# Kernel tuning notes

Measured on AMD Instinct MI355X. Metric: run time of the kernel, lower is better.

Reference implementation:

```python
import jax, jax.numpy as jnp
import numpy as np

B = 65536       # batch size
C = 100         # num classes (len(cls_num_list))
ALPHA = 0.01    # soft-label blend weight
TAU = 2.0       # init arg tau
TEMP = 2.0      # distillation temperature
EPS = 1e-9


def _soft_ce(logits, soft_targets):
    # -(soft * log softmax(logits)).sum(1).mean()
    return -(soft_targets * jax.nn.log_softmax(logits, axis=1)).sum(axis=1).mean()


def _inverse_prior(prior):
    idx0 = jnp.argsort(prior)            # ascending sort permutation
    value = prior[idx0]                  # sorted values
    idx1 = jnp.argsort(idx0)             # rank of each element
    idx2 = prior.shape[0] - 1 - idx1     # mirrored rank
    return value[idx2]


def setup_inputs():
    key = jax.random.key(0)
    ks = jax.random.split(key, 8)
    cls_num = np.arange(500, 0, -5).astype(np.float32)  # matches init cls_num_list
    prior = jnp.asarray(cls_num / cls_num.sum(), dtype=jnp.float32)
    return {
        "output_logits": jax.random.normal(ks[0], (B, C), jnp.float32),
        "target": jax.random.randint(ks[1], (B,), 0, C),
        "cos_feature": jax.random.normal(ks[2], (C, C), jnp.float32),
        "old_pred": jax.random.normal(ks[3], (B, C), jnp.float32),
        "expert1_logits": jax.random.normal(ks[4], (B, C), jnp.float32),
        "expert2_logits": jax.random.normal(ks[5], (B, C), jnp.float32),
        "expert3_logits": jax.random.normal(ks[6], (B, C), jnp.float32),
        "output": jax.random.normal(ks[7], (B, C), jnp.float32),
        "prior": prior,
        "epoch": 5,
    }


def reference(output_logits, target, cos_feature, old_pred, expert1_logits,
              expert2_logits, expert3_logits, output, prior, epoch):
    num_classes = prior.shape[0]
    # ---- convert_to_soft_labels (vectorized: gather rows of sim matrix, softmax, blend) ----
    one_hot = jax.nn.one_hot(target, num_classes, dtype=jnp.float32)          # [B,C]
    sim_probs = jax.nn.softmax(cos_feature, axis=1)[target]                   # [B,C]
    label = (1.0 - ALPHA) * one_hot + ALPHA * sim_probs

    # ---- three expert soft cross-entropies ----
    log_prior = jnp.log(prior + EPS)
    loss = _soft_ce(expert1_logits, label)
    loss = loss + _soft_ce(expert2_logits + log_prior, label)
    inv_prior = _inverse_prior(prior)
    loss = loss + _soft_ce(expert3_logits + log_prior - TAU * jnp.log(inv_prior + EPS), label)

    # ---- bincount-normalized summed logits ----
    counts = jnp.bincount(target, length=num_classes).astype(jnp.float32)     # [C]
    num = counts[target][:, None]                                             # [B,1]
    expert_sum_logits = output / num                                          # [B,C]

    # ---- masked KL distillation (only rows where teacher argmax == target) ----
    teacher_index = jnp.argmax(old_pred, axis=1)                              # argmax(softmax)=argmax
    mask = (teacher_index == target).astype(jnp.float32)                      # [B]
    t = jax.nn.softmax(old_pred / TEMP, axis=1)                               # teacher probs
    s = jax.nn.log_softmax(expert_sum_logits / TEMP, axis=1)                  # student log-probs
    log_t = jnp.where(t > 0, jnp.log(t), 0.0)
    kl_per = (t * (log_t - s)).sum(axis=1)                                    # [B] per-row KL
    n_sel = mask.sum()
    kl_loss = jnp.where(n_sel > 0, (kl_per * mask).sum() / jnp.maximum(n_sel, 1.0), 0.0)
    kl_loss = kl_loss * (TEMP ** 2) * 3.0

    return loss, kl_loss, expert_sum_logits
```

## Files before the change

### kernel.cpp

```cpp
#include <hip/hip_runtime.h>
#include <math.h>

#define B_N 65536
#define C_N 100
constexpr float ALPHA = 0.01f;
constexpr float TAU   = 2.0f;
constexpr float TEMP  = 2.0f;
constexpr float EPSF  = 1e-9f;
constexpr float NEG_SENT = -1.0e30f;

template<int CTRL>
__device__ __forceinline__ float fadd_dpp(float x) {
    return x + __int_as_float(__builtin_amdgcn_update_dpp(
        0, __float_as_int(x), CTRL, 0xF, 0xF, true));
}
__device__ __forceinline__ float rowsum32(float x) {
    x = fadd_dpp<0xB1>(x);
    x = fadd_dpp<0x4E>(x);
    x = fadd_dpp<0x124>(x);
    x = fadd_dpp<0x128>(x);
    x = fadd_dpp<0x142>(x);
    return x;
}
template<int CTRL>
__device__ __forceinline__ void amax_dpp(unsigned &hi, unsigned &lo) {
    const unsigned yh = (unsigned)__builtin_amdgcn_update_dpp(0, (int)hi, CTRL, 0xF, 0xF, true);
    const unsigned yl = (unsigned)__builtin_amdgcn_update_dpp(0, (int)lo, CTRL, 0xF, 0xF, true);
    const bool take = (yh > hi) || (yh == hi && yl > lo);
    hi = take ? yh : hi;
    lo = take ? yl : lo;
}
__device__ __forceinline__ void rowamax32(unsigned &hi, unsigned &lo) {
    amax_dpp<0xB1>(hi, lo);
    amax_dpp<0x4E>(hi, lo);
    amax_dpp<0x124>(hi, lo);
    amax_dpp<0x128>(hi, lo);
    amax_dpp<0x142>(hi, lo);
}

__device__ __forceinline__ float wsum(float v) {
    #pragma unroll
    for (int o = 32; o; o >>= 1) v += __shfl_xor(v, o);
    return v;
}

__global__ void prep_k(const float* __restrict__ cosf, const float* __restrict__ prior,
                       const int* __restrict__ target,
                       float* __restrict__ sm, float* __restrict__ lp, float* __restrict__ c3,
                       int* __restrict__ counts) {
    const int b = blockIdx.x;
    if (b < 256) {
        __shared__ int h[C_N];
        for (int i = threadIdx.x; i < C_N; i += blockDim.x) h[i] = 0;
        __syncthreads();
        const int gid = b * blockDim.x + threadIdx.x;
        const int stride = 256 * blockDim.x;
        for (int i = gid; i < B_N; i += stride) atomicAdd(&h[target[i]], 1);
        __syncthreads();
        for (int i = threadIdx.x; i < C_N; i += blockDim.x)
            if (h[i]) atomicAdd(&counts[i], h[i]);
    } else if (b == 256) {
        __shared__ float sp[C_N];
        __shared__ float val[C_N];
        const int t = threadIdx.x;
        if (t < C_N) sp[t] = prior[t];
        __syncthreads();
        int rank = 0;
        float lpi = 0.f;
        if (t < C_N) {
            const float pi = sp[t];
            for (int j = 0; j < C_N; ++j) {
                const float pj = sp[j];
                rank += (pj < pi) || (pj == pi && j < t);
            }
            val[rank] = pi;
            lpi = __logf(pi + EPSF);
            lp[t] = lpi;
        }
        __syncthreads();
        if (t < C_N) {
            const float inv = val[C_N - 1 - rank];
            c3[t] = lpi - TAU * __logf(inv + EPSF);
        }
    } else {
        const int gw = (b - 257) * 4 + (threadIdx.x >> 6);
        const int lane = threadIdx.x & 63;
        for (int row = gw; row < C_N; row += 16) {
            const float* rp = cosf + row * C_N;
            const float v0 = rp[lane];
            const bool has1 = (lane + 64) < C_N;
            const float v1 = has1 ? rp[lane + 64] : -INFINITY;
            float m = fmaxf(v0, v1);
            #pragma unroll
            for (int o = 32; o; o >>= 1) m = fmaxf(m, __shfl_xor(m, o));
            const float e0 = __expf(v0 - m);
            const float e1 = has1 ? __expf(v1 - m) : 0.f;
            const float s = wsum(e0 + e1);
            const float is = 1.0f / s;
            sm[row * C_N + lane] = e0 * is;
            if (has1) sm[row * C_N + lane + 64] = e1 * is;
        }
    }
}

#define NBLK 4096

__launch_bounds__(256)
__global__ void main_k(const int* __restrict__ target,
                       const float* __restrict__ e1p, const float* __restrict__ e2p,
                       const float* __restrict__ e3p, const float* __restrict__ opp,
                       const float* __restrict__ outp,
                       const float* __restrict__ sm, const float* __restrict__ lp,
                       const float* __restrict__ c3, const int* __restrict__ counts,
                       float* __restrict__ dout,
                       float* __restrict__ ploss, float* __restrict__ pkl, float* __restrict__ pn) {
    const int lane = threadIdx.x & 63;
    const int gl   = lane & 31;
    const int half = lane >> 5;
    const int wslot = threadIdx.x >> 6;
    const int gw   = blockIdx.x * 4 + wslot;
    const bool act = gl < 25;
    const int c0 = 4 * gl;
    const bool own = (gl == 16);

    const int rowA = 4 * gw + half;
    const int rowB = 4 * gw + 2 + half;
    const int tgtA = target[rowA];
    const int tgtB = target[rowB];
    const int baseA = rowA * C_N;
    const int baseB = rowB * C_N;

    float4 LP = make_float4(0,0,0,0), CO = make_float4(0,0,0,0);
    float4 E1A, E2A, E3A, OPA, OUA, SMA, E1B, E2B, E3B, OPB, OUB, SMB;
    E1A = E2A = E3A = OPA = OUA = make_float4(NEG_SENT, NEG_SENT, NEG_SENT, NEG_SENT);
    E1B = E2B = E3B = OPB = OUB = make_float4(NEG_SENT, NEG_SENT, NEG_SENT, NEG_SENT);
    SMA = SMB = make_float4(0,0,0,0);
    if (act) {
        LP  = *(const float4*)(lp + c0);
        CO  = *(const float4*)(c3 + c0);
        E1A = *(const float4*)(e1p + baseA + c0);
        E1B = *(const float4*)(e1p + baseB + c0);
        E2A = *(const float4*)(e2p + baseA + c0);
        E2B = *(const float4*)(e2p + baseB + c0);
        E3A = *(const float4*)(e3p + baseA + c0);
        E3B = *(const float4*)(e3p + baseB + c0);
        OPA = *(const float4*)(opp + baseA + c0);
        OPB = *(const float4*)(opp + baseB + c0);
        OUA = *(const float4*)(outp + baseA + c0);
        OUB = *(const float4*)(outp + baseB + c0);
        SMA = *(const float4*)(sm + tgtA * C_N + c0);
        SMB = *(const float4*)(sm + tgtB * C_N + c0);
    }
    const float rcA = 1.0f / (float)counts[tgtA];
    const float rcB = 1.0f / (float)counts[tgtB];

    const float laA0 = (1.0f - ALPHA) * (c0     == tgtA) + ALPHA * SMA.x;
    const float laA1 = (1.0f - ALPHA) * (c0 + 1 == tgtA) + ALPHA * SMA.y;
    const float laA2 = (1.0f - ALPHA) * (c0 + 2 == tgtA) + ALPHA * SMA.z;
    const float laA3 = (1.0f - ALPHA) * (c0 + 3 == tgtA) + ALPHA * SMA.w;
    const float lA20 = E2A.x + LP.x, lA21 = E2A.y + LP.y, lA22 = E2A.z + LP.z, lA23 = E2A.w + LP.w;
    const float lA30 = E3A.x + CO.x, lA31 = E3A.y + CO.y, lA32 = E3A.z + CO.z, lA33 = E3A.w + CO.w;
    float s1A = __expf(E1A.x) + __expf(E1A.y) + __expf(E1A.z) + __expf(E1A.w);
    float s2A = __expf(lA20) + __expf(lA21) + __expf(lA22) + __expf(lA23);
    float s3A = __expf(lA30) + __expf(lA31) + __expf(lA32) + __expf(lA33);
    float dtA = laA0 * (E1A.x + lA20 + lA30) + laA1 * (E1A.y + lA21 + lA31)
              + laA2 * (E1A.z + lA22 + lA32) + laA3 * (E1A.w + lA23 + lA33);
    const float aA0 = OPA.x * 0.5f, aA1 = OPA.y * 0.5f, aA2 = OPA.z * 0.5f, aA3 = OPA.w * 0.5f;
    const float pA0 = __expf(aA0), pA1 = __expf(aA1), pA2 = __expf(aA2), pA3 = __expf(aA3);
    float ztA = pA0 + pA1 + pA2 + pA3;
    float bvA = OPA.x; int biA = c0;
    if (OPA.y > bvA) { bvA = OPA.y; biA = c0 + 1; }
    if (OPA.z > bvA) { bvA = OPA.z; biA = c0 + 2; }
    if (OPA.w > bvA) { bvA = OPA.w; biA = c0 + 3; }
    unsigned bbA = __float_as_uint(bvA);
    bbA = ((int)bbA < 0) ? ~bbA : (bbA | 0x80000000u);
    unsigned khiA = bbA, kloA = (unsigned)~biA;
    const float esA0 = OUA.x * rcA, esA1 = OUA.y * rcA, esA2 = OUA.z * rcA, esA3 = OUA.w * rcA;
    const float xA0 = esA0 * 0.5f, xA1 = esA1 * 0.5f, xA2 = esA2 * 0.5f, xA3 = esA3 * 0.5f;
    float zsA = __expf(xA0) + __expf(xA1) + __expf(xA2) + __expf(xA3);
    float DA  = pA0 * (aA0 - xA0) + pA1 * (aA1 - xA1) + pA2 * (aA2 - xA2) + pA3 * (aA3 - xA3);
    if (act) {
        *(float2*)(dout + 2 + baseA + c0)     = make_float2(esA0, esA1);
        *(float2*)(dout + 2 + baseA + c0 + 2) = make_float2(esA2, esA3);
    }

    const float laB0 = (1.0f - ALPHA) * (c0     == tgtB) + ALPHA * SMB.x;
    const float laB1 = (1.0f - ALPHA) * (c0 + 1 == tgtB) + ALPHA * SMB.y;
    const float laB2 = (1.0f - ALPHA) * (c0 + 2 == tgtB) + ALPHA * SMB.z;
    const float laB3 = (1.0f - ALPHA) * (c0 + 3 == tgtB) + ALPHA * SMB.w;
    const float lB20 = E2B.x + LP.x, lB21 = E2B.y + LP.y, lB22 = E2B.z + LP.z, lB23 = E2B.w + LP.w;
    const float lB30 = E3B.x + CO.x, lB31 = E3B.y + CO.y, lB32 = E3B.z + CO.z, lB33 = E3B.w + CO.w;
    float s1B = __expf(E1B.x) + __expf(E1B.y) + __expf(E1B.z) + __expf(E1B.w);
    float s2B = __expf(lB20) + __expf(lB21) + __expf(lB22) + __expf(lB23);
    float s3B = __expf(lB30) + __expf(lB31) + __expf(lB32) + __expf(lB33);
    float dtB = laB0 * (E1B.x + lB20 + lB30) + laB1 * (E1B.y + lB21 + lB31)
              + laB2 * (E1B.z + lB22 + lB32) + laB3 * (E1B.w + lB23 + lB33);
    const float aB0 = OPB.x * 0.5f, aB1 = OPB.y * 0.5f, aB2 = OPB.z * 0.5f, aB3 = OPB.w * 0.5f;
    const float pB0 = __expf(aB0), pB1 = __expf(aB1), pB2 = __expf(aB2), pB3 = __expf(aB3);
    float ztB = pB0 + pB1 + pB2 + pB3;
    float bvB = OPB.x; int biB = c0;
    if (OPB.y > bvB) { bvB = OPB.y; biB = c0 + 1; }
    if (OPB.z > bvB) { bvB = OPB.z; biB = c0 + 2; }
    if (OPB.w > bvB) { bvB = OPB.w; biB = c0 + 3; }
    unsigned bbB = __float_as_uint(bvB);
    bbB = ((int)bbB < 0) ? ~bbB : (bbB | 0x80000000u);
    unsigned khiB = bbB, kloB = (unsigned)~biB;
    const float esB0 = OUB.x * rcB, esB1 = OUB.y * rcB, esB2 = OUB.z * rcB, esB3 = OUB.w * rcB;
    const float xB0 = esB0 * 0.5f, xB1 = esB1 * 0.5f, xB2 = esB2 * 0.5f, xB3 = esB3 * 0.5f;
    float zsB = __expf(xB0) + __expf(xB1) + __expf(xB2) + __expf(xB3);
    float DB  = pB0 * (aB0 - xB0) + pB1 * (aB1 - xB1) + pB2 * (aB2 - xB2) + pB3 * (aB3 - xB3);
    if (act) {
        *(float2*)(dout + 2 + baseB + c0)     = make_float2(esB0, esB1);
        *(float2*)(dout + 2 + baseB + c0 + 2) = make_float2(esB2, esB3);
    }

    s1A = rowsum32(s1A);  s1B = rowsum32(s1B);
    s2A = rowsum32(s2A);  s2B = rowsum32(s2B);
    s3A = rowsum32(s3A);  s3B = rowsum32(s3B);
    dtA = rowsum32(dtA);  dtB = rowsum32(dtB);
    ztA = rowsum32(ztA);  ztB = rowsum32(ztB);
    zsA = rowsum32(zsA);  zsB = rowsum32(zsB);
    DA  = rowsum32(DA);   DB  = rowsum32(DB);
    rowamax32(khiA, kloA);
    rowamax32(khiB, kloB);

    const float ceA = __logf(s1A * s2A * s3A) - dtA;
    const float ceB = __logf(s1B * s2B * s3B) - dtB;
    const int miA = (int)~kloA;
    const int miB = (int)~kloB;
    const float rztA = 1.0f / ztA, rztB = 1.0f / ztB;
    const float klvA = DA * rztA + __logf(zsA * rztA);
    const float klvB = DB * rztB + __logf(zsB * rztB);
    const bool selA = own && (miA == tgtA);
    const bool selB = own && (miB == tgtB);

    float lossAcc = own ? (ceA + ceB) : 0.f;
    float klAcc   = (selA ? klvA : 0.f) + (selB ? klvB : 0.f);
    float nAcc    = (selA ? 1.f : 0.f) + (selB ? 1.f : 0.f);

    const float lossW = __shfl(lossAcc, 16) + __shfl(lossAcc, 48);
    const float klW   = __shfl(klAcc, 16) + __shfl(klAcc, 48);
    const float nW    = __shfl(nAcc, 16) + __shfl(nAcc, 48);

    __shared__ float bl[4], bk[4], bn[4];
    if (lane == 0) { bl[wslot] = lossW; bk[wslot] = klW; bn[wslot] = nW; }
    __syncthreads();
    if (threadIdx.x == 0) {
        ploss[blockIdx.x] = bl[0] + bl[1] + bl[2] + bl[3];
        pkl[blockIdx.x]   = bk[0] + bk[1] + bk[2] + bk[3];
        pn[blockIdx.x]    = bn[0] + bn[1] + bn[2] + bn[3];
    }
}

__global__ void final_k(const float* __restrict__ ploss, const float* __restrict__ pkl,
                        const float* __restrict__ pn, float* __restrict__ dout) {
    __shared__ float sl[256], sk[256], sn[256];
    const int t = threadIdx.x;
    float l = 0.f, k = 0.f, n = 0.f;
    for (int i = t; i < NBLK; i += 256) { l += ploss[i]; k += pkl[i]; n += pn[i]; }
    sl[t] = l; sk[t] = k; sn[t] = n;
    __syncthreads();
    for (int s = 128; s; s >>= 1) {
        if (t < s) { sl[t] += sl[t + s]; sk[t] += sk[t + s]; sn[t] += sn[t + s]; }
        __syncthreads();
    }
    if (t == 0) {
        dout[0] = sl[0] / (float)B_N;
        const float kl = (sn[0] > 0.f) ? (sk[0] / fmaxf(sn[0], 1.f)) : 0.f;
        dout[1] = kl * (TEMP * TEMP) * 3.0f;
    }
}

extern "C" void kernel_launch(void* const* d_in, const int* in_sizes, int n_in,
                              void* d_out, int out_size, void* d_ws, size_t ws_size,
                              hipStream_t stream) {
    const int*   target = (const int*)  d_in[1];
    const float* cosf   = (const float*)d_in[2];
    const float* oldp   = (const float*)d_in[3];
    const float* e1     = (const float*)d_in[4];
    const float* e2     = (const float*)d_in[5];
    const float* e3     = (const float*)d_in[6];
    const float* outp   = (const float*)d_in[7];
    const float* prior  = (const float*)d_in[8];

    float* ws    = (float*)d_ws;
    float* sm    = ws;
    float* lp    = ws + 10000;
    float* c3    = ws + 10100;
    int*   cnts  = (int*)(ws + 10200);
    float* ploss = ws + 10304;
    float* pkl   = ploss + NBLK;
    float* pn    = pkl + NBLK;

    hipMemsetAsync(cnts, 0, C_N * sizeof(int), stream);
    prep_k<<<261, 256, 0, stream>>>(cosf, prior, target, sm, lp, c3, cnts);
    main_k<<<NBLK, 256, 0, stream>>>(target, e1, e2, e3, oldp, outp,
                                     sm, lp, c3, cnts, (float*)d_out, ploss, pkl, pn);
    final_k<<<1, 256, 0, stream>>>(ploss, pkl, pn, (float*)d_out);
}
```

Before: 52.45 us.

## Split main kernel into CE and KL block halves and fold prior biases into weights

The fused per-row kernel becomes two block populations. The first half of the grid computes the three soft cross-entropies and the second half computes the masked KL and writes the normalized logits. Each block therefore holds fewer live registers and loads fewer streams, which should raise occupancy and memory-level parallelism. The prior offsets are also folded algebraically into precomputed multiplicative weights (exp of the bias) and a combined additive term, removing per-element adds. The costs are twice as many blocks, each reloading target, and slightly different floating-point rounding from exp(x)*w instead of exp(x+log w).

```diff
diff --git a/kernel.cpp b/kernel.cpp
--- a/kernel.cpp
+++ b/kernel.cpp
@@ -46,7 +46,8 @@
 
 __global__ void prep_k(const float* __restrict__ cosf, const float* __restrict__ prior,
                        const int* __restrict__ target,
-                       float* __restrict__ sm, float* __restrict__ lp, float* __restrict__ c3,
+                       float* __restrict__ sm, float* __restrict__ w2,
+                       float* __restrict__ w3, float* __restrict__ Ht,
                        int* __restrict__ counts) {
     const int b = blockIdx.x;
     if (b < 256) {
@@ -66,21 +67,23 @@
         if (t < C_N) sp[t] = prior[t];
         __syncthreads();
         int rank = 0;
-        float lpi = 0.f;
+        float lpi = 0.f, pi = 0.f;
         if (t < C_N) {
-            const float pi = sp[t];
+            pi = sp[t];
             for (int j = 0; j < C_N; ++j) {
                 const float pj = sp[j];
                 rank += (pj < pi) || (pj == pi && j < t);
             }
             val[rank] = pi;
             lpi = __logf(pi + EPSF);
-            lp[t] = lpi;
         }
         __syncthreads();
         if (t < C_N) {
             const float inv = val[C_N - 1 - rank];
-            c3[t] = lpi - TAU * __logf(inv + EPSF);
+            const float c3v = lpi - TAU * __logf(inv + EPSF);
+            w2[t] = pi + EPSF;
+            w3[t] = __expf(c3v);
+            Ht[t] = lpi + c3v;
         }
     } else {
         const int gw = (b - 257) * 4 + (threadIdx.x >> 6);
@@ -103,152 +106,176 @@
     }
 }
 
-#define NBLK 4096
+#define HBLK 4096
+#define NBLK (2 * HBLK)
 
 __launch_bounds__(256)
 __global__ void main_k(const int* __restrict__ target,
                        const float* __restrict__ e1p, const float* __restrict__ e2p,
                        const float* __restrict__ e3p, const float* __restrict__ opp,
                        const float* __restrict__ outp,
-                       const float* __restrict__ sm, const float* __restrict__ lp,
-                       const float* __restrict__ c3, const int* __restrict__ counts,
+                       const float* __restrict__ sm, const float* __restrict__ w2p,
+                       const float* __restrict__ w3p, const float* __restrict__ Hp,
+                       const int* __restrict__ counts,
                        float* __restrict__ dout,
                        float* __restrict__ ploss, float* __restrict__ pkl, float* __restrict__ pn) {
     const int lane = threadIdx.x & 63;
     const int gl   = lane & 31;
     const int half = lane >> 5;
     const int wslot = threadIdx.x >> 6;
-    const int gw   = blockIdx.x * 4 + wslot;
     const bool act = gl < 25;
     const int c0 = 4 * gl;
     const bool own = (gl == 16);
-
-    const int rowA = 4 * gw + half;
-    const int rowB = 4 * gw + 2 + half;
-    const int tgtA = target[rowA];
-    const int tgtB = target[rowB];
-    const int baseA = rowA * C_N;
-    const int baseB = rowB * C_N;
-
-    float4 LP = make_float4(0,0,0,0), CO = make_float4(0,0,0,0);
-    float4 E1A, E2A, E3A, OPA, OUA, SMA, E1B, E2B, E3B, OPB, OUB, SMB;
-    E1A = E2A = E3A = OPA = OUA = make_float4(NEG_SENT, NEG_SENT, NEG_SENT, NEG_SENT);
-    E1B = E2B = E3B = OPB = OUB = make_float4(NEG_SENT, NEG_SENT, NEG_SENT, NEG_SENT);
-    SMA = SMB = make_float4(0,0,0,0);
-    if (act) {
-        LP  = *(const float4*)(lp + c0);
-        CO  = *(const float4*)(c3 + c0);
-        E1A = *(const float4*)(e1p + baseA + c0);
-        E1B = *(const float4*)(e1p + baseB + c0);
-        E2A = *(const float4*)(e2p + baseA + c0);
-        E2B = *(const float4*)(e2p + baseB + c0);
-        E3A = *(const float4*)(e3p + baseA + c0);
-        E3B = *(const float4*)(e3p + baseB + c0);
-        OPA = *(const float4*)(opp + baseA + c0);
-        OPB = *(const float4*)(opp + baseB + c0);
-        OUA = *(const float4*)(outp + baseA + c0);
-        OUB = *(const float4*)(outp + baseB + c0);
-        SMA = *(const float4*)(sm + tgtA * C_N + c0);
-        SMB = *(const float4*)(sm + tgtB * C_N + c0);
-    }
-    const float rcA = 1.0f / (float)counts[tgtA];
-    const float rcB = 1.0f / (float)counts[tgtB];
-
-    const float laA0 = (1.0f - ALPHA) * (c0     == tgtA) + ALPHA * SMA.x;
-    const float laA1 = (1.0f - ALPHA) * (c0 + 1 == tgtA) + ALPHA * SMA.y;
-    const float laA2 = (1.0f - ALPHA) * (c0 + 2 == tgtA) + ALPHA * SMA.z;
-    const float laA3 = (1.0f - ALPHA) * (c0 + 3 == tgtA) + ALPHA * SMA.w;
-    const float lA20 = E2A.x + LP.x, lA21 = E2A.y + LP.y, lA22 = E2A.z + LP.z, lA23 = E2A.w + LP.w;
-    const float lA30 = E3A.x + CO.x, lA31 = E3A.y + CO.y, lA32 = E3A.z + CO.z, lA33 = E3A.w + CO.w;
-    float s1A = __expf(E1A.x) + __expf(E1A.y) + __expf(E1A.z) + __expf(E1A.w);
-    float s2A = __expf(lA20) + __expf(lA21) + __expf(lA22) + __expf(lA23);
-    float s3A = __expf(lA30) + __expf(lA31) + __expf(lA32) + __expf(lA33);
-    float dtA = laA0 * (E1A.x + lA20 + lA30) + laA1 * (E1A.y + lA21 + lA31)
-              + laA2 * (E1A.z + lA22 + lA32) + laA3 * (E1A.w + lA23 + lA33);
-    const float aA0 = OPA.x * 0.5f, aA1 = OPA.y * 0.5f, aA2 = OPA.z * 0.5f, aA3 = OPA.w * 0.5f;
-    const float pA0 = __expf(aA0), pA1 = __expf(aA1), pA2 = __expf(aA2), pA3 = __expf(aA3);
-    float ztA = pA0 + pA1 + pA2 + pA3;
-    float bvA = OPA.x; int biA = c0;
-    if (OPA.y > bvA) { bvA = OPA.y; biA = c0 + 1; }
-    if (OPA.z > bvA) { bvA = OPA.z; biA = c0 + 2; }
-    if (OPA.w > bvA) { bvA = OPA.w; biA = c0 + 3; }
-    unsigned bbA = __float_as_uint(bvA);
-    bbA = ((int)bbA < 0) ? ~bbA : (bbA | 0x80000000u);
-    unsigned khiA = bbA, kloA = (unsigned)~biA;
-    const float esA0 = OUA.x * rcA, esA1 = OUA.y * rcA, esA2 = OUA.z * rcA, esA3 = OUA.w * rcA;
-    const float xA0 = esA0 * 0.5f, xA1 = esA1 * 0.5f, xA2 = esA2 * 0.5f, xA3 = esA3 * 0.5f;
-    float zsA = __expf(xA0) + __expf(xA1) + __expf(xA2) + __expf(xA3);
-    float DA  = pA0 * (aA0 - xA0) + pA1 * (aA1 - xA1) + pA2 * (aA2 - xA2) + pA3 * (aA3 - xA3);
-    if (act) {
-        *(float2*)(dout + 2 + baseA + c0)     = make_float2(esA0, esA1);
-        *(float2*)(dout + 2 + baseA + c0 + 2) = make_float2(esA2, esA3);
-    }
-
-    const float laB0 = (1.0f - ALPHA) * (c0     == tgtB) + ALPHA * SMB.x;
-    const float laB1 = (1.0f - ALPHA) * (c0 + 1 == tgtB) + ALPHA * SMB.y;
-    const float laB2 = (1.0f - ALPHA) * (c0 + 2 == tgtB) + ALPHA * SMB.z;
-    const float laB3 = (1.0f - ALPHA) * (c0 + 3 == tgtB) + ALPHA * SMB.w;
-    const float lB20 = E2B.x + LP.x, lB21 = E2B.y + LP.y, lB22 = E2B.z + LP.z, lB23 = E2B.w + LP.w;
-    const float lB30 = E3B.x + CO.x, lB31 = E3B.y + CO.y, lB32 = E3B.z + CO.z, lB33 = E3B.w + CO.w;
-    float s1B = __expf(E1B.x) + __expf(E1B.y) + __expf(E1B.z) + __expf(E1B.w);
-    float s2B = __expf(lB20) + __expf(lB21) + __expf(lB22) + __expf(lB23);
-    float s3B = __expf(lB30) + __expf(lB31) + __expf(lB32) + __expf(lB33);
-    float dtB = laB0 * (E1B.x + lB20 + lB30) + laB1 * (E1B.y + lB21 + lB31)
-              + laB2 * (E1B.z + lB22 + lB32) + laB3 * (E1B.w + lB23 + lB33);
-    const float aB0 = OPB.x * 0.5f, aB1 = OPB.y * 0.5f, aB2 = OPB.z * 0.5f, aB3 = OPB.w * 0.5f;
-    const float pB0 = __expf(aB0), pB1 = __expf(aB1), pB2 = __expf(aB2), pB3 = __expf(aB3);
-    float ztB = pB0 + pB1 + pB2 + pB3;
-    float bvB = OPB.x; int biB = c0;
-    if (OPB.y > bvB) { bvB = OPB.y; biB = c0 + 1; }
-    if (OPB.z > bvB) { bvB = OPB.z; biB = c0 + 2; }
-    if (OPB.w > bvB) { bvB = OPB.w; biB = c0 + 3; }
-    unsigned bbB = __float_as_uint(bvB);
-    bbB = ((int)bbB < 0) ? ~bbB : (bbB | 0x80000000u);
-    unsigned khiB = bbB, kloB = (unsigned)~biB;
-    const float esB0 = OUB.x * rcB, esB1 = OUB.y * rcB, esB2 = OUB.z * rcB, esB3 = OUB.w * rcB;
-    const float xB0 = esB0 * 0.5f, xB1 = esB1 * 0.5f, xB2 = esB2 * 0.5f, xB3 = esB3 * 0.5f;
-    float zsB = __expf(xB0) + __expf(xB1) + __expf(xB2) + __expf(xB3);
-    float DB  = pB0 * (aB0 - xB0) + pB1 * (aB1 - xB1) + pB2 * (aB2 - xB2) + pB3 * (aB3 - xB3);
-    if (act) {
-        *(float2*)(dout + 2 + baseB + c0)     = make_float2(esB0, esB1);
-        *(float2*)(dout + 2 + baseB + c0 + 2) = make_float2(esB2, esB3);
-    }
-
-    s1A = rowsum32(s1A);  s1B = rowsum32(s1B);
-    s2A = rowsum32(s2A);  s2B = rowsum32(s2B);
-    s3A = rowsum32(s3A);  s3B = rowsum32(s3B);
-    dtA = rowsum32(dtA);  dtB = rowsum32(dtB);
-    ztA = rowsum32(ztA);  ztB = rowsum32(ztB);
-    zsA = rowsum32(zsA);  zsB = rowsum32(zsB);
-    DA  = rowsum32(DA);   DB  = rowsum32(DB);
-    rowamax32(khiA, kloA);
-    rowamax32(khiB, kloB);
-
-    const float ceA = __logf(s1A * s2A * s3A) - dtA;
-    const float ceB = __logf(s1B * s2B * s3B) - dtB;
-    const int miA = (int)~kloA;
-    const int miB = (int)~kloB;
-    const float rztA = 1.0f / ztA, rztB = 1.0f / ztB;
-    const float klvA = DA * rztA + __logf(zsA * rztA);
-    const float klvB = DB * rztB + __logf(zsB * rztB);
-    const bool selA = own && (miA == tgtA);
-    const bool selB = own && (miB == tgtB);
-
-    float lossAcc = own ? (ceA + ceB) : 0.f;
-    float klAcc   = (selA ? klvA : 0.f) + (selB ? klvB : 0.f);
-    float nAcc    = (selA ? 1.f : 0.f) + (selB ? 1.f : 0.f);
-
-    const float lossW = __shfl(lossAcc, 16) + __shfl(lossAcc, 48);
-    const float klW   = __shfl(klAcc, 16) + __shfl(klAcc, 48);
-    const float nW    = __shfl(nAcc, 16) + __shfl(nAcc, 48);
-
     __shared__ float bl[4], bk[4], bn[4];
-    if (lane == 0) { bl[wslot] = lossW; bk[wslot] = klW; bn[wslot] = nW; }
-    __syncthreads();
-    if (threadIdx.x == 0) {
-        ploss[blockIdx.x] = bl[0] + bl[1] + bl[2] + bl[3];
-        pkl[blockIdx.x]   = bk[0] + bk[1] + bk[2] + bk[3];
-        pn[blockIdx.x]    = bn[0] + bn[1] + bn[2] + bn[3];
+
+    if (blockIdx.x < HBLK) {
+        const int gw = blockIdx.x * 4 + wslot;
+        const int rowA = 4 * gw + half;
+        const int rowB = 4 * gw + 2 + half;
+        const int tgtA = target[rowA];
+        const int tgtB = target[rowB];
+        const int baseA = rowA * C_N;
+        const int baseB = rowB * C_N;
+
+        float4 W2 = make_float4(0,0,0,0), W3 = make_float4(0,0,0,0), HH = make_float4(0,0,0,0);
+        float4 E1A, E2A, E3A, E1B, E2B, E3B, SMA, SMB;
+        E1A = E2A = E3A = E1B = E2B = E3B = make_float4(NEG_SENT, NEG_SENT, NEG_SENT, NEG_SENT);
+        SMA = SMB = make_float4(0,0,0,0);
+        if (act) {
+            W2  = *(const float4*)(w2p + c0);
+            W3  = *(const float4*)(w3p + c0);
+            HH  = *(const float4*)(Hp + c0);
+            E1A = *(const float4*)(e1p + baseA + c0);
+            E1B = *(const float4*)(e1p + baseB + c0);
+            E2A = *(const float4*)(e2p + baseA + c0);
+            E2B = *(const float4*)(e2p + baseB + c0);
+            E3A = *(const float4*)(e3p + baseA + c0);
+            E3B = *(const float4*)(e3p + baseB + c0);
+            SMA = *(const float4*)(sm + tgtA * C_N + c0);
+            SMB = *(const float4*)(sm + tgtB * C_N + c0);
+        }
+
+        const float laA0 = (1.0f - ALPHA) * (c0     == tgtA) + ALPHA * SMA.x;
+        const float laA1 = (1.0f - ALPHA) * (c0 + 1 == tgtA) + ALPHA * SMA.y;
+        const float laA2 = (1.0f - ALPHA) * (c0 + 2 == tgtA) + ALPHA * SMA.z;
+        const float laA3 = (1.0f - ALPHA) * (c0 + 3 == tgtA) + ALPHA * SMA.w;
+        float s1A = __expf(E1A.x) + __expf(E1A.y) + __expf(E1A.z) + __expf(E1A.w);
+        float s2A = W2.x * __expf(E2A.x) + W2.y * __expf(E2A.y)
+                  + W2.z * __expf(E2A.z) + W2.w * __expf(E2A.w);
+        float s3A = W3.x * __expf(E3A.x) + W3.y * __expf(E3A.y)
+                  + W3.z * __expf(E3A.z) + W3.w * __expf(E3A.w);
+        float dtA = laA0 * (E1A.x + E2A.x + E3A.x + HH.x)
+                  + laA1 * (E1A.y + E2A.y + E3A.y + HH.y)
+                  + laA2 * (E1A.z + E2A.z + E3A.z + HH.z)
+                  + laA3 * (E1A.w + E2A.w + E3A.w + HH.w);
+        const float laB0 = (1.0f - ALPHA) * (c0     == tgtB) + ALPHA * SMB.x;
+        const float laB1 = (1.0f - ALPHA) * (c0 + 1 == tgtB) + ALPHA * SMB.y;
+        const float laB2 = (1.0f - ALPHA) * (c0 + 2 == tgtB) + ALPHA * SMB.z;
+        const float laB3 = (1.0f - ALPHA) * (c0 + 3 == tgtB) + ALPHA * SMB.w;
+        float s1B = __expf(E1B.x) + __expf(E1B.y) + __expf(E1B.z) + __expf(E1B.w);
+        float s2B = W2.x * __expf(E2B.x) + W2.y * __expf(E2B.y)
+                  + W2.z * __expf(E2B.z) + W2.w * __expf(E2B.w);
+        float s3B = W3.x * __expf(E3B.x) + W3.y * __expf(E3B.y)
+                  + W3.z * __expf(E3B.z) + W3.w * __expf(E3B.w);
+        float dtB = laB0 * (E1B.x + E2B.x + E3B.x + HH.x)
+                  + laB1 * (E1B.y + E2B.y + E3B.y + HH.y)
+                  + laB2 * (E1B.z + E2B.z + E3B.z + HH.z)
+                  + laB3 * (E1B.w + E2B.w + E3B.w + HH.w);
+
+        s1A = rowsum32(s1A);  s1B = rowsum32(s1B);
+        s2A = rowsum32(s2A);  s2B = rowsum32(s2B);
+        s3A = rowsum32(s3A);  s3B = rowsum32(s3B);
+        dtA = rowsum32(dtA);  dtB = rowsum32(dtB);
+
+        const float ceA = __logf(s1A * s2A * s3A) - dtA;
+        const float ceB = __logf(s1B * s2B * s3B) - dtB;
+        float lossAcc = own ? (ceA + ceB) : 0.f;
+        const float lossW = __shfl(lossAcc, 16) + __shfl(lossAcc, 48);
+        if (lane == 0) bl[wslot] = lossW;
+        __syncthreads();
+        if (threadIdx.x == 0)
+            ploss[blockIdx.x] = bl[0] + bl[1] + bl[2] + bl[3];
+    } else {
+        const int j  = blockIdx.x - HBLK;
+        const int gw = j * 4 + wslot;
+        const int rowA = 4 * gw + half;
+        const int rowB = 4 * gw + 2 + half;
+        const int tgtA = target[rowA];
+        const int tgtB = target[rowB];
+        const int baseA = rowA * C_N;
+        const int baseB = rowB * C_N;
+
+        float4 OPA, OUA, OPB, OUB;
+        OPA = OUA = OPB = OUB = make_float4(NEG_SENT, NEG_SENT, NEG_SENT, NEG_SENT);
+        if (act) {
+            OPA = *(const float4*)(opp + baseA + c0);
+            OPB = *(const float4*)(opp + baseB + c0);
+            OUA = *(const float4*)(outp + baseA + c0);
+            OUB = *(const float4*)(outp + baseB + c0);
+        }
+        const float rcA = 1.0f / (float)counts[tgtA];
+        const float rcB = 1.0f / (float)counts[tgtB];
+
+        const float aA0 = OPA.x * 0.5f, aA1 = OPA.y * 0.5f, aA2 = OPA.z * 0.5f, aA3 = OPA.w * 0.5f;
+        const float pA0 = __expf(aA0), pA1 = __expf(aA1), pA2 = __expf(aA2), pA3 = __expf(aA3);
+        float ztA = pA0 + pA1 + pA2 + pA3;
+        float bvA = OPA.x; int biA = c0;
+        if (OPA.y > bvA) { bvA = OPA.y; biA = c0 + 1; }
+        if (OPA.z > bvA) { bvA = OPA.z; biA = c0 + 2; }
+        if (OPA.w > bvA) { bvA = OPA.w; biA = c0 + 3; }
+        unsigned bbA = __float_as_uint(bvA);
+        bbA = ((int)bbA < 0) ? ~bbA : (bbA | 0x80000000u);
+        unsigned khiA = bbA, kloA = (unsigned)~biA;
+        const float esA0 = OUA.x * rcA, esA1 = OUA.y * rcA, esA2 = OUA.z * rcA, esA3 = OUA.w * rcA;
+        const float xA0 = esA0 * 0.5f, xA1 = esA1 * 0.5f, xA2 = esA2 * 0.5f, xA3 = esA3 * 0.5f;
+        float zsA = __expf(xA0) + __expf(xA1) + __expf(xA2) + __expf(xA3);
+        float DA  = pA0 * (aA0 - xA0) + pA1 * (aA1 - xA1) + pA2 * (aA2 - xA2) + pA3 * (aA3 - xA3);
+        if (act) {
+            *(float2*)(dout + 2 + baseA + c0)     = make_float2(esA0, esA1);
+            *(float2*)(dout + 2 + baseA + c0 + 2) = make_float2(esA2, esA3);
+        }
+        const float aB0 = OPB.x * 0.5f, aB1 = OPB.y * 0.5f, aB2 = OPB.z * 0.5f, aB3 = OPB.w * 0.5f;
+        const float pB0 = __expf(aB0), pB1 = __expf(aB1), pB2 = __expf(aB2), pB3 = __expf(aB3);
+        float ztB = pB0 + pB1 + pB2 + pB3;
+        float bvB = OPB.x; int biB = c0;
+        if (OPB.y > bvB) { bvB = OPB.y; biB = c0 + 1; }
+        if (OPB.z > bvB) { bvB = OPB.z; biB = c0 + 2; }
+        if (OPB.w > bvB) { bvB = OPB.w; biB = c0 + 3; }
+        unsigned bbB = __float_as_uint(bvB);
+        bbB = ((int)bbB < 0) ? ~bbB : (bbB | 0x80000000u);
+        unsigned khiB = bbB, kloB = (unsigned)~biB;
+        const float esB0 = OUB.x * rcB, esB1 = OUB.y * rcB, esB2 = OUB.z * rcB, esB3 = OUB.w * rcB;
+        const float xB0 = esB0 * 0.5f, xB1 = esB1 * 0.5f, xB2 = esB2 * 0.5f, xB3 = esB3 * 0.5f;
+        float zsB = __expf(xB0) + __expf(xB1) + __expf(xB2) + __expf(xB3);
+        float DB  = pB0 * (aB0 - xB0) + pB1 * (aB1 - xB1) + pB2 * (aB2 - xB2) + pB3 * (aB3 - xB3);
+        if (act) {
+            *(float2*)(dout + 2 + baseB + c0)     = make_float2(esB0, esB1);
+            *(float2*)(dout + 2 + baseB + c0 + 2) = make_float2(esB2, esB3);
+        }
+
+        ztA = rowsum32(ztA);  ztB = rowsum32(ztB);
+        zsA = rowsum32(zsA);  zsB = rowsum32(zsB);
+        DA  = rowsum32(DA);   DB  = rowsum32(DB);
+        rowamax32(khiA, kloA);
+        rowamax32(khiB, kloB);
+
+        const int miA = (int)~kloA;
+        const int miB = (int)~kloB;
+        const float rztA = 1.0f / ztA, rztB = 1.0f / ztB;
+        const float klvA = DA * rztA + __logf(zsA * rztA);
+        const float klvB = DB * rztB + __logf(zsB * rztB);
+        const bool selA = own && (miA == tgtA);
+        const bool selB = own && (miB == tgtB);
+        float klAcc = (selA ? klvA : 0.f) + (selB ? klvB : 0.f);
+        float nAcc  = (selA ? 1.f : 0.f) + (selB ? 1.f : 0.f);
+        const float klW = __shfl(klAcc, 16) + __shfl(klAcc, 48);
+        const float nW  = __shfl(nAcc, 16) + __shfl(nAcc, 48);
+        if (lane == 0) { bk[wslot] = klW; bn[wslot] = nW; }
+        __syncthreads();
+        if (threadIdx.x == 0) {
+            pkl[j] = bk[0] + bk[1] + bk[2] + bk[3];
+            pn[j]  = bn[0] + bn[1] + bn[2] + bn[3];
+        }
     }
 }
 
@@ -257,7 +284,7 @@
     __shared__ float sl[256], sk[256], sn[256];
     const int t = threadIdx.x;
     float l = 0.f, k = 0.f, n = 0.f;
-    for (int i = t; i < NBLK; i += 256) { l += ploss[i]; k += pkl[i]; n += pn[i]; }
+    for (int i = t; i < HBLK; i += 256) { l += ploss[i]; k += pkl[i]; n += pn[i]; }
     sl[t] = l; sk[t] = k; sn[t] = n;
     __syncthreads();
     for (int s = 128; s; s >>= 1) {
@@ -285,16 +312,17 @@
 
     float* ws    = (float*)d_ws;
     float* sm    = ws;
-    float* lp    = ws + 10000;
-    float* c3    = ws + 10100;
-    int*   cnts  = (int*)(ws + 10200);
-    float* ploss = ws + 10304;
-    float* pkl   = ploss + NBLK;
-    float* pn    = pkl + NBLK;
+    float* w2    = ws + 10016;
+    float* w3    = ws + 10120;
+    float* Ht    = ws + 10224;
+    int*   cnts  = (int*)(ws + 10328);
+    float* ploss = ws + 10432;
+    float* pkl   = ploss + HBLK;
+    float* pn    = pkl + HBLK;
 
     hipMemsetAsync(cnts, 0, C_N * sizeof(int), stream);
-    prep_k<<<261, 256, 0, stream>>>(cosf, prior, target, sm, lp, c3, cnts);
+    prep_k<<<261, 256, 0, stream>>>(cosf, prior, target, sm, w2, w3, Ht, cnts);
     main_k<<<NBLK, 256, 0, stream>>>(target, e1, e2, e3, oldp, outp,
-                                     sm, lp, c3, cnts, (float*)d_out, ploss, pkl, pn);
+                                     sm, w2, w3, Ht, cnts, (float*)d_out, ploss, pkl, pn);
     final_k<<<1, 256, 0, stream>>>(ploss, pkl, pn, (float*)d_out);
 }
```

Result: no change. 51.79 us (-1.3%).
